# Optimization experiments

Hardware: AMD Instinct MI355X
Metric: run time of the kernel (lower is better)

The kernel has to match this reference:

```python
import jax, jax.numpy as jnp
import numpy as np

DT = 0.1


def _gru_step(x, h, wih, whh, bih, bhh):
    # x: [B,R,I], h: [B,R,H], wih: [R,3H,I], whh: [R,3H,H]
    H = h.shape[-1]
    gi = jnp.einsum('bri,rji->brj', x, wih) + bih
    gh = jnp.einsum('brh,rjh->brj', h, whh) + bhh
    i_r, i_z, i_n = gi[..., :H], gi[..., H:2 * H], gi[..., 2 * H:]
    h_r, h_z, h_n = gh[..., :H], gh[..., H:2 * H], gh[..., 2 * H:]
    reset = jax.nn.sigmoid(i_r + h_r)
    update = jax.nn.sigmoid(i_z + h_z)
    new = jnp.tanh(i_n + reset * h_n)
    return (1 - update) * new + update * h


def _flow(state, cond, gsw, gsb, gcw, lw, lb, ow, ob):
    # gated-relaxation FINDR-style flow, R parallel MLPs (einsum 'bri,roi->bro')
    gate = jax.nn.sigmoid(jnp.einsum('bri,roi->bro', state, gsw) + gsb
                          + jnp.einsum('bri,roi->bro', cond, gcw))
    h = jnp.concatenate([state, cond], axis=-1)          # [B,R,2L]
    h = jax.nn.silu(jnp.einsum('bri,roi->bro', h, lw) + lb)
    target = jnp.tanh(jnp.einsum('bri,roi->bro', h, ow) + ob)
    return gate * (-state + target)


def setup_inputs() -> dict:
    key = jax.random.key(0)
    B, R, L, M, Hh, Hf, T = 64, 12, 32, 16, 32, 64, 200
    pairs = [(s, t) for s in range(R) for t in range(R) if s != t]
    E = len(pairs)  # 132 directed inter-region edges
    src_idx = jnp.array([s for s, _ in pairs], dtype=jnp.int32)
    tgt_idx = jnp.array([t for _, t in pairs], dtype=jnp.int32)
    ks = jax.random.split(key, 12)

    def xav(k, shape):
        fan = shape[-1] + shape[-2]
        return jax.random.normal(k, shape, jnp.float32) * np.sqrt(2.0 / fan)

    return {
        'z0': jax.random.normal(ks[0], (B, R, L), jnp.float32),
        'h0': jax.random.normal(ks[1], (B, R, Hh), jnp.float32),
        'mean_w': xav(ks[2], (E, M, L)),
        'mean_b': jnp.zeros((E, M), jnp.float32),
        'add_w': 0.1 * jax.random.normal(ks[3], (E, L, M), jnp.float32),
        'gate_state_w': xav(ks[4], (R, L, L)),
        'gate_state_b': jnp.zeros((R, L), jnp.float32),
        'gate_cond_w': xav(ks[5], (R, L, L)),
        'layer_w': xav(ks[6], (R, Hf, 2 * L)),
        'layer_b': jnp.zeros((R, Hf), jnp.float32),
        'out_w': xav(ks[7], (R, L, Hf)),
        'out_b': jnp.zeros((R, L), jnp.float32),
        'wih': xav(ks[8], (R, 3 * Hh, L)),
        'whh': xav(ks[9], (R, 3 * Hh, Hh)),
        'bih': jnp.zeros((R, 3 * Hh), jnp.float32),
        'bhh': jnp.zeros((R, 3 * Hh), jnp.float32),
        'src_idx': src_idx,
        'tgt_idx': tgt_idx,
        'n_steps': T,
    }


def reference(z0, h0, mean_w, mean_b, add_w,
              gate_state_w, gate_state_b, gate_cond_w,
              layer_w, layer_b, out_w, out_b,
              wih, whh, bih, bhh, src_idx, tgt_idx, n_steps):
    def step(carry, _):
        z, h = carry
        src = z[:, src_idx]                                   # gather [B,E,L]
        mean = jnp.einsum('bes,ems->bem', src, mean_w) + mean_b  # edge messages
        add = jnp.einsum('bem,elm->bel', mean, add_w)         # [B,E,L]
        inc_add = jnp.zeros_like(z).at[:, tgt_idx].add(add)   # scatter-add -> [B,R,L]
        drift = _flow(z, inc_add, gate_state_w, gate_state_b, gate_cond_w,
                      layer_w, layer_b, out_w, out_b)
        h_new = _gru_step(inc_add, h, wih, whh, bih, bhh)
        z_new = z + DT * drift
        return (z_new, h_new), (z_new, mean)

    (z_f, h_f), (z_traj, msgs) = jax.lax.scan(step, (z0, h0), None, length=n_steps)
    # z_traj: [T,B,R,L] -> [B,T,R,L]; msgs: [T,B,E,M] -> [B,T,E,M]
    return z_traj.transpose(1, 0, 2, 3), h_f, msgs.transpose(1, 0, 2, 3)
```

## Files before the change

### kernel.cpp

```cpp
#include <hip/hip_runtime.h>


constexpr int R  = 12;
constexpr int L  = 32;
constexpr int M  = 16;
constexpr int HH = 32;
constexpr int HF = 64;
constexpr int E  = 132;
constexpr int G3 = 96;
constexpr float DT = 0.1f;

constexpr int G  = 4;
constexpr int BS = 512;

typedef float f4v __attribute__((ext_vector_type(4)));

__device__ __forceinline__ float sigmoidf(float x) {
    return 1.0f / (1.0f + __expf(-x));
}
__device__ __forceinline__ float fma4(float4 a, float4 x, float acc) {
    acc = fmaf(a.x, x.x, acc);
    acc = fmaf(a.y, x.y, acc);
    acc = fmaf(a.z, x.z, acc);
    return fmaf(a.w, x.w, acc);
}

__device__ __forceinline__ void sync_lds() {
    asm volatile("s_waitcnt lgkmcnt(0)" ::: "memory");
    __builtin_amdgcn_s_barrier();
    asm volatile("" ::: "memory");
}

__global__ __launch_bounds__(BS)
__attribute__((amdgpu_waves_per_eu(2, 2)))
void nv_main(
    const float* __restrict__ z0,     const float* __restrict__ h0,
    const float* __restrict__ mean_w, const float* __restrict__ mean_b,
    const float* __restrict__ add_w,
    const float* __restrict__ gsw,    const float* __restrict__ gsb,
    const float* __restrict__ gcw,
    const float* __restrict__ lw,     const float* __restrict__ lb,
    const float* __restrict__ ow_w,   const float* __restrict__ ob,
    const float* __restrict__ wih,    const float* __restrict__ whh,
    const float* __restrict__ bih,    const float* __restrict__ bhh,
    const int* __restrict__ src_idx,  const int* __restrict__ tgt_idx,
    const int* __restrict__ n_steps_p,
    float* __restrict__ zx,
    float* __restrict__ out, int B)
{
    const int r   = blockIdx.x;
    const int grp = blockIdx.y;
    const int tid = threadIdx.x;
    const int T   = n_steps_p[0];
    const int b0  = grp * G;
    const size_t ZXN = (size_t)B * (R * L);

    float* __restrict__ out_z    = out;
    float* __restrict__ out_hf   = out + (size_t)B * T * R * L;
    float* __restrict__ out_msgs = out_hf + (size_t)B * R * HH;

    __shared__ __align__(16) float wadd_s[11 * L * M];
    __shared__ __align__(16) float wih_s[G3 * L];
    __shared__ __align__(16) float zS[G * R * L];
    __shared__ __align__(16) float hSS[G * HH];
    __shared__ __align__(16) float meanS[G * 11 * M];
    __shared__ __align__(16) float incS[G * L];
    __shared__ __align__(16) float gateS[G * L];
    __shared__ __align__(16) float shSS[G * HF];
    __shared__ __align__(16) float giSS[G * G3];
    __shared__ __align__(16) float ghSS[G * G3];
    __shared__ int edgeE[11], edgeSrc[11];

    if (tid == 0) {
        int c = 0;
        for (int e = 0; e < E; ++e)
            if (tgt_idx[e] == r) { edgeE[c] = e; edgeSrc[c] = src_idx[e]; ++c; }
    }
    __syncthreads();

    float4 wbuf[32];
    float biasA = 0.f, biasB = 0.f, biasC = 0.f;

    if (tid < 176) {
        const int el = tid >> 4, m = tid & 15;
        const int row = edgeE[el] * M + m;
        const float4* p = (const float4*)(mean_w + (size_t)row * L);
#pragma unroll
        for (int k = 0; k < 8; ++k) wbuf[k] = p[k];
        biasA = mean_b[row];
    }
    if (tid >= 192 && tid < 288) {
        const int j = tid - 192, row = r * G3 + j;
        const float4* p = (const float4*)(whh + (size_t)row * HH);
#pragma unroll
        for (int k = 0; k < 8; ++k) wbuf[k] = p[k];
        biasA = bhh[row];
    }
    if (tid < 256) {
        const int j = tid & 63, row = r * HF + j;
        const float4* p = (const float4*)(lw + (size_t)row * 2 * L);
#pragma unroll
        for (int k = 0; k < 16; ++k) wbuf[8 + k] = p[k];
        biasB = lb[row];
    }
    if (tid >= 256 && tid < 384) {
        const int j = (tid - 256) & 31, row = r * L + j;
        const float4* pa = (const float4*)(gsw + (size_t)row * L);
        const float4* pb = (const float4*)(gcw + (size_t)row * L);
#pragma unroll
        for (int k = 0; k < 8; ++k) { wbuf[8 + k] = pa[k]; wbuf[16 + k] = pb[k]; }
        biasB = gsb[row];
    }
    if (tid >= 384) {
        const int j = (tid - 384) & 31, row = r * L + j;
        const float4* p = (const float4*)(ow_w + (size_t)row * HF);
#pragma unroll
        for (int k = 0; k < 16; ++k) wbuf[8 + k] = p[k];
        biasB = ob[row];
    }
    if (tid >= 128) {
        const int j = (tid - 128) % 96;
        biasC = bih[r * G3 + j];
    }

    for (int i = tid; i < 11 * L * M; i += BS) {
        const int e = i >> 9, rem = i & 511, l = rem >> 4, m = rem & 15;
        wadd_s[((e * 4 + (m >> 2)) * 32 + l) * 4 + (m & 3)] =
            add_w[((size_t)edgeE[e] * L + l) * M + m];
    }
    for (int i = tid; i < G3 * L; i += BS)
        wih_s[i] = wih[(size_t)r * G3 * L + i];

    for (int i = tid; i < G * R * L; i += BS) {
        const int g = i / (R * L), rl = i - g * (R * L);
        zS[i] = z0[(size_t)(b0 + g) * R * L + rl];
    }
    for (int i = tid; i < G * HH; i += BS) {
        const int g = i >> 5, hh = i & 31;
        hSS[i] = h0[(size_t)(b0 + g) * R * HH + r * HH + hh];
    }
    __syncthreads();

    const float NANF = __uint_as_float(0xFFFFFFFFu);

    for (int t = 0; t < T; ++t) {
        if (tid < 176) {
            const int sr = edgeSrc[tid >> 4];
#pragma unroll
            for (int g = 0; g < G; ++g) {
                const float4* zp = (const float4*)(zS + g * (R * L) + sr * L);
                float a = biasA;
#pragma unroll
                for (int c = 0; c < 8; ++c) a = fma4(wbuf[c], zp[c], a);
                meanS[g * 176 + tid] = a;
            }
        } else if (tid >= 192 && tid < 288) {
            const int j = tid - 192;
#pragma unroll
            for (int g = 0; g < G; ++g) {
                const float4* hp = (const float4*)(hSS + g * HH);
                float a = biasA;
#pragma unroll
                for (int c = 0; c < 8; ++c) a = fma4(wbuf[c], hp[c], a);
                ghSS[g * G3 + j] = a;
            }
        } else if (tid >= 480 && t >= 1) {
            float* __restrict__ zq = zx + (size_t)((t - 1) % 3) * ZXN;
            const int i = tid - 480;
            const int g = i >> 3, l4 = i & 7;
            float* pp = zq + (size_t)(b0 + g) * (R * L) + r * L + l4 * 4;
#pragma unroll
            for (int w = 0; w < 4; ++w)
                __hip_atomic_store(pp + w, NANF, __ATOMIC_RELAXED,
                                   __HIP_MEMORY_SCOPE_AGENT);
        }
        sync_lds();

        if (tid < 128) {
            const int g = tid >> 5;
            const float4* mp = (const float4*)(meanS + g * 176);
            const float4* wp = (const float4*)wadd_s;
            const int l = tid & 31;
            float a = 0.f;
#pragma unroll
            for (int e = 0; e < 11; ++e)
#pragma unroll
                for (int c = 0; c < 4; ++c)
                    a = fma4(wp[(e * 4 + c) * 32 + l], mp[e * 4 + c], a);
            incS[tid] = a;
        } else if (tid < 304) {
            const int k = tid - 128;
            const int g = k / 44, i = k - g * 44;
            const int el = i >> 2, m4 = i & 3;
            const f4v v = *(const f4v*)(meanS + g * 176 + i * 4);
            __builtin_nontemporal_store(
                v, (f4v*)&out_msgs[((size_t)(b0 + g) * T + t) * (E * M)
                                   + edgeE[el] * 16 + m4 * 4]);
        } else if (tid >= 448) {
            asm volatile("s_waitcnt vmcnt(0)" ::: "memory");
        }
        sync_lds();

        if (tid < 256) {
            const int j = tid & 63, g = tid >> 6;
            const float4* zp = (const float4*)(zS + g * (R * L) + r * L);
            const float4* ip = (const float4*)(incS + g * L);
            float a = biasB;
#pragma unroll
            for (int c = 0; c < 8; ++c) {
                a = fma4(wbuf[8 + c], zp[c], a);
                a = fma4(wbuf[16 + c], ip[c], a);
            }
            shSS[g * HF + j] = a * sigmoidf(a);
        } else if (tid < 384) {
            const int k = tid - 256;
            const int j = k & 31, g = k >> 5;
            const float4* zp = (const float4*)(zS + g * (R * L) + r * L);
            const float4* ip = (const float4*)(incS + g * L);
            float a = biasB;
#pragma unroll
            for (int c = 0; c < 8; ++c) {
                a = fma4(wbuf[8 + c], zp[c], a);
                a = fma4(wbuf[16 + c], ip[c], a);
            }
            gateS[g * L + j] = sigmoidf(a);
        }
        if (tid >= 128) {
            const int k = tid - 128;
            const int j = k % 96, g = k / 96;
            const float4* wp = (const float4*)wih_s + j * 8;
            const float4* ip = (const float4*)(incS + g * L);
            float a = biasC;
#pragma unroll
            for (int c = 0; c < 8; ++c) a = fma4(wp[c], ip[c], a);
            giSS[g * G3 + j] = a;
        }
        sync_lds();

        float* __restrict__ zxp = zx + (size_t)((t + 1) % 3) * ZXN;
        if (tid >= 384) {
            const int k = tid - 384;
            const int j = k & 31, g = k >> 5;
            const float4* sp = (const float4*)(shSS + g * HF);
            float a = biasB;
#pragma unroll
            for (int c = 0; c < 16; ++c) a = fma4(wbuf[8 + c], sp[c], a);
            const float target = tanhf(a);
            const float zv = zS[g * (R * L) + r * L + j];
            const float znew = zv + DT * gateS[g * L + j] * (target - zv);
            zS[g * (R * L) + r * L + j] = znew;
            if (t + 1 < T)
                __hip_atomic_store(&zxp[(size_t)(b0 + g) * (R * L) + r * L + j],
                                   znew, __ATOMIC_RELAXED,
                                   __HIP_MEMORY_SCOPE_AGENT);
            __builtin_nontemporal_store(
                znew, &out_z[((size_t)(b0 + g) * T + t) * (R * L) + r * L + j]);
        } else {
            if (tid >= 256) {
                const int i = tid - 256;
                const int g = i >> 5, hh = i & 31;
                const float ir  = giSS[g * G3 + hh];
                const float iz  = giSS[g * G3 + HH + hh];
                const float inn = giSS[g * G3 + 2 * HH + hh];
                const float hr  = ghSS[g * G3 + hh];
                const float hz  = ghSS[g * G3 + HH + hh];
                const float hnv = ghSS[g * G3 + 2 * HH + hh];
                const float reset = sigmoidf(ir + hr);
                const float upd   = sigmoidf(iz + hz);
                const float nw    = tanhf(inn + reset * hnv);
                hSS[g * HH + hh] = (1.0f - upd) * nw + upd * hSS[g * HH + hh];
            }
            if (tid < 352 && t + 1 < T) {
                const int team = tid >> 5, rem = tid & 31;
                const int s    = team + (team >= r ? 1 : 0);
                const int g    = rem >> 3, l4 = rem & 7;
                const float* sp =
                    zxp + (size_t)(b0 + g) * (R * L) + s * L + l4 * 4;
                float4 v;
                for (;;) {
                    v.x = __hip_atomic_load(sp + 0, __ATOMIC_RELAXED, __HIP_MEMORY_SCOPE_AGENT);
                    v.y = __hip_atomic_load(sp + 1, __ATOMIC_RELAXED, __HIP_MEMORY_SCOPE_AGENT);
                    v.z = __hip_atomic_load(sp + 2, __ATOMIC_RELAXED, __HIP_MEMORY_SCOPE_AGENT);
                    v.w = __hip_atomic_load(sp + 3, __ATOMIC_RELAXED, __HIP_MEMORY_SCOPE_AGENT);
                    if (v.x == v.x && v.y == v.y && v.z == v.z && v.w == v.w)
                        break;
                    __builtin_amdgcn_s_sleep(1);
                }
                ((float4*)zS)[g * (R * L / 4) + s * (L / 4) + l4] = v;
            }
        }
        sync_lds();
    }

    for (int i = tid; i < G * HH; i += BS) {
        const int g = i >> 5, hh = i & 31;
        __builtin_nontemporal_store(
            hSS[i], &out_hf[(size_t)(b0 + g) * R * HH + r * HH + hh]);
    }
}

extern "C" void kernel_launch(void* const* d_in, const int* in_sizes, int n_in,
                              void* d_out, int out_size, void* d_ws, size_t ws_size,
                              hipStream_t stream) {
    const float* z0     = (const float*)d_in[0];
    const float* h0     = (const float*)d_in[1];
    const float* mean_w = (const float*)d_in[2];
    const float* mean_b = (const float*)d_in[3];
    const float* add_w  = (const float*)d_in[4];
    const float* gsw    = (const float*)d_in[5];
    const float* gsb    = (const float*)d_in[6];
    const float* gcw    = (const float*)d_in[7];
    const float* lw     = (const float*)d_in[8];
    const float* lb     = (const float*)d_in[9];
    const float* ow_w   = (const float*)d_in[10];
    const float* ob     = (const float*)d_in[11];
    const float* wih    = (const float*)d_in[12];
    const float* whh    = (const float*)d_in[13];
    const float* bih    = (const float*)d_in[14];
    const float* bhh    = (const float*)d_in[15];
    const int* src_idx  = (const int*)d_in[16];
    const int* tgt_idx  = (const int*)d_in[17];
    const int* n_steps  = (const int*)d_in[18];

    const int B  = in_sizes[0] / (R * L);
    const int NG = B / G;

    float* zx = (float*)d_ws;

    (void)hipMemsetAsync(zx, 0xFF, (size_t)3 * B * R * L * sizeof(float), stream);

    nv_main<<<dim3(R, NG), dim3(BS), 72000, stream>>>(
        z0, h0, mean_w, mean_b, add_w, gsw, gsb, gcw, lw, lb, ow_w, ob,
        wih, whh, bih, bhh, src_idx, tgt_idx, n_steps,
        zx, (float*)d_out, B);
}
```

Baseline: 1.048 ms.

## Pad and swizzle LDS layouts and rebalance edge-message and GRU work across threads

Pads the per-region rows of the shared z buffer and the incoming-message buffer to 36 floats and XOR-swizzles the wih rows in shared memory, to reduce LDS bank conflicts on float4 reads. It also spreads the edge-message mat-vec over 352 threads, two batch rows each, instead of 176 threads doing four. The recurrent hidden-state projection moves from the first phase into the second phase on threads 384-479. This lengthens the critical path less per step but changes phase occupancy and register allocation.

```diff
diff --git a/kernel.cpp b/kernel.cpp
--- a/kernel.cpp
+++ b/kernel.cpp
@@ -12,6 +12,9 @@
 
 constexpr int G  = 4;
 constexpr int BS = 512;
+constexpr int ZR = 36;
+constexpr int ZG = R * ZR;
+constexpr int IS = 36;
 
 typedef float f4v __attribute__((ext_vector_type(4)));
 
@@ -61,10 +64,10 @@
 
     __shared__ __align__(16) float wadd_s[11 * L * M];
     __shared__ __align__(16) float wih_s[G3 * L];
-    __shared__ __align__(16) float zS[G * R * L];
+    __shared__ __align__(16) float zS[G * ZG];
     __shared__ __align__(16) float hSS[G * HH];
     __shared__ __align__(16) float meanS[G * 11 * M];
-    __shared__ __align__(16) float incS[G * L];
+    __shared__ __align__(16) float incS[G * IS];
     __shared__ __align__(16) float gateS[G * L];
     __shared__ __align__(16) float shSS[G * HF];
     __shared__ __align__(16) float giSS[G * G3];
@@ -81,16 +84,17 @@
     float4 wbuf[32];
     float biasA = 0.f, biasB = 0.f, biasC = 0.f;
 
-    if (tid < 176) {
-        const int el = tid >> 4, m = tid & 15;
+    if (tid < 352) {
+        const int rowl = tid % 176;
+        const int el = rowl >> 4, m = rowl & 15;
         const int row = edgeE[el] * M + m;
         const float4* p = (const float4*)(mean_w + (size_t)row * L);
 #pragma unroll
         for (int k = 0; k < 8; ++k) wbuf[k] = p[k];
         biasA = mean_b[row];
     }
-    if (tid >= 192 && tid < 288) {
-        const int j = tid - 192, row = r * G3 + j;
+    if (tid >= 384 && tid < 480) {
+        const int j = tid - 384, row = r * G3 + j;
         const float4* p = (const float4*)(whh + (size_t)row * HH);
 #pragma unroll
         for (int k = 0; k < 8; ++k) wbuf[k] = p[k];
@@ -128,12 +132,15 @@
         wadd_s[((e * 4 + (m >> 2)) * 32 + l) * 4 + (m & 3)] =
             add_w[((size_t)edgeE[e] * L + l) * M + m];
     }
-    for (int i = tid; i < G3 * L; i += BS)
-        wih_s[i] = wih[(size_t)r * G3 * L + i];
+    for (int i = tid; i < G3 * L; i += BS) {
+        const int j = i >> 5, cw = i & 31, c = cw >> 2, w = cw & 3;
+        wih_s[j * 32 + ((c ^ (j & 7)) << 2) + w] = wih[(size_t)r * G3 * L + i];
+    }
 
     for (int i = tid; i < G * R * L; i += BS) {
         const int g = i / (R * L), rl = i - g * (R * L);
-        zS[i] = z0[(size_t)(b0 + g) * R * L + rl];
+        const int room = rl >> 5, l = rl & 31;
+        zS[g * ZG + room * ZR + l] = z0[(size_t)(b0 + g) * R * L + rl];
     }
     for (int i = tid; i < G * HH; i += BS) {
         const int g = i >> 5, hh = i & 31;
@@ -144,25 +151,18 @@
     const float NANF = __uint_as_float(0xFFFFFFFFu);
 
     for (int t = 0; t < T; ++t) {
-        if (tid < 176) {
-            const int sr = edgeSrc[tid >> 4];
-#pragma unroll
-            for (int g = 0; g < G; ++g) {
-                const float4* zp = (const float4*)(zS + g * (R * L) + sr * L);
+        if (tid < 352) {
+            const int rowl = tid % 176;
+            const int sr = edgeSrc[rowl >> 4];
+            const int gb = (tid < 176) ? 0 : 2;
+#pragma unroll
+            for (int gg = 0; gg < 2; ++gg) {
+                const int g = gb + gg;
+                const float4* zp = (const float4*)(zS + g * ZG + sr * ZR);
                 float a = biasA;
 #pragma unroll
                 for (int c = 0; c < 8; ++c) a = fma4(wbuf[c], zp[c], a);
-                meanS[g * 176 + tid] = a;
-            }
-        } else if (tid >= 192 && tid < 288) {
-            const int j = tid - 192;
-#pragma unroll
-            for (int g = 0; g < G; ++g) {
-                const float4* hp = (const float4*)(hSS + g * HH);
-                float a = biasA;
-#pragma unroll
-                for (int c = 0; c < 8; ++c) a = fma4(wbuf[c], hp[c], a);
-                ghSS[g * G3 + j] = a;
+                meanS[g * 176 + rowl] = a;
             }
         } else if (tid >= 480 && t >= 1) {
             float* __restrict__ zq = zx + (size_t)((t - 1) % 3) * ZXN;
@@ -177,17 +177,16 @@
         sync_lds();
 
         if (tid < 128) {
-            const int g = tid >> 5;
+            const int g = tid >> 5, l = tid & 31;
             const float4* mp = (const float4*)(meanS + g * 176);
             const float4* wp = (const float4*)wadd_s;
-            const int l = tid & 31;
             float a = 0.f;
 #pragma unroll
             for (int e = 0; e < 11; ++e)
 #pragma unroll
                 for (int c = 0; c < 4; ++c)
                     a = fma4(wp[(e * 4 + c) * 32 + l], mp[e * 4 + c], a);
-            incS[tid] = a;
+            incS[g * IS + l] = a;
         } else if (tid < 304) {
             const int k = tid - 128;
             const int g = k / 44, i = k - g * 44;
@@ -196,15 +195,25 @@
             __builtin_nontemporal_store(
                 v, (f4v*)&out_msgs[((size_t)(b0 + g) * T + t) * (E * M)
                                    + edgeE[el] * 16 + m4 * 4]);
-        } else if (tid >= 448) {
+        } else if (tid >= 384 && tid < 480) {
+            const int j = tid - 384;
+#pragma unroll
+            for (int g = 0; g < G; ++g) {
+                const float4* hp = (const float4*)(hSS + g * HH);
+                float a = biasA;
+#pragma unroll
+                for (int c = 0; c < 8; ++c) a = fma4(wbuf[c], hp[c], a);
+                ghSS[g * G3 + j] = a;
+            }
+        } else if (tid >= 480) {
             asm volatile("s_waitcnt vmcnt(0)" ::: "memory");
         }
         sync_lds();
 
         if (tid < 256) {
             const int j = tid & 63, g = tid >> 6;
-            const float4* zp = (const float4*)(zS + g * (R * L) + r * L);
-            const float4* ip = (const float4*)(incS + g * L);
+            const float4* zp = (const float4*)(zS + g * ZG + r * ZR);
+            const float4* ip = (const float4*)(incS + g * IS);
             float a = biasB;
 #pragma unroll
             for (int c = 0; c < 8; ++c) {
@@ -215,8 +224,8 @@
         } else if (tid < 384) {
             const int k = tid - 256;
             const int j = k & 31, g = k >> 5;
-            const float4* zp = (const float4*)(zS + g * (R * L) + r * L);
-            const float4* ip = (const float4*)(incS + g * L);
+            const float4* zp = (const float4*)(zS + g * ZG + r * ZR);
+            const float4* ip = (const float4*)(incS + g * IS);
             float a = biasB;
 #pragma unroll
             for (int c = 0; c < 8; ++c) {
@@ -228,11 +237,13 @@
         if (tid >= 128) {
             const int k = tid - 128;
             const int j = k % 96, g = k / 96;
-            const float4* wp = (const float4*)wih_s + j * 8;
-            const float4* ip = (const float4*)(incS + g * L);
+            const float* wb = wih_s + j * 32;
+            const int jx = j & 7;
+            const float4* ip = (const float4*)(incS + g * IS);
             float a = biasC;
 #pragma unroll
-            for (int c = 0; c < 8; ++c) a = fma4(wp[c], ip[c], a);
+            for (int c = 0; c < 8; ++c)
+                a = fma4(*(const float4*)(wb + ((c ^ jx) << 2)), ip[c], a);
             giSS[g * G3 + j] = a;
         }
         sync_lds();
@@ -246,9 +257,9 @@
 #pragma unroll
             for (int c = 0; c < 16; ++c) a = fma4(wbuf[8 + c], sp[c], a);
             const float target = tanhf(a);
-            const float zv = zS[g * (R * L) + r * L + j];
+            const float zv = zS[g * ZG + r * ZR + j];
             const float znew = zv + DT * gateS[g * L + j] * (target - zv);
-            zS[g * (R * L) + r * L + j] = znew;
+            zS[g * ZG + r * ZR + j] = znew;
             if (t + 1 < T)
                 __hip_atomic_store(&zxp[(size_t)(b0 + g) * (R * L) + r * L + j],
                                    znew, __ATOMIC_RELAXED,
@@ -286,7 +297,7 @@
                         break;
                     __builtin_amdgcn_s_sleep(1);
                 }
-                ((float4*)zS)[g * (R * L / 4) + s * (L / 4) + l4] = v;
+                *(float4*)(zS + g * ZG + s * ZR + l4 * 4) = v;
             }
         }
         sync_lds();
```

Result: faster. 903.1 us (-13.8%).
